# Optimization experiments

Hardware: AMD Instinct MI355X
Metric: run time of the kernel (lower is better)

## Reference

```python
import jax, jax.numpy as jnp
import numpy as np

C_S = 128
C_T = 128
C_OUT = 128


def _proj(x, W, b):
    # 1x1x1 Conv3d == per-voxel linear over channel dim. x: [B, Cin, T, H, W]
    return jnp.einsum('oc,bcthw->bothw', W, x) + b[None, :, None, None, None]


def setup_inputs() -> dict:
    key = jax.random.key(0)
    ks = jax.random.split(key, 12)
    B, T, H, W = 4, 4, 32, 32
    spatial_features = jax.random.normal(ks[0], (B, T, C_S, H, W), dtype=jnp.float32)
    temporal_features = jax.random.normal(ks[1], (B, C_T, T, H, W), dtype=jnp.float32)
    def w(k, o, i):
        return jax.random.normal(k, (o, i), dtype=jnp.float32) * (i ** -0.5)
    return {
        'spatial_features': spatial_features,
        'temporal_features': temporal_features,
        'Wq': w(ks[2], C_OUT, C_S), 'bq': jnp.zeros((C_OUT,), jnp.float32),
        'Wk': w(ks[3], C_OUT, C_T), 'bk': jnp.zeros((C_OUT,), jnp.float32),
        'Wv': w(ks[4], C_OUT, C_T), 'bv': jnp.zeros((C_OUT,), jnp.float32),
        'Wo': w(ks[5], C_OUT, C_OUT), 'bo': jnp.zeros((C_OUT,), jnp.float32),
    }


def reference(spatial_features, temporal_features, Wq, bq, Wk, bk, Wv, bv, Wo, bo):
    B, T, C_s, H, W = spatial_features.shape
    N = T * H * W
    scale = C_OUT ** -0.5
    # permute(0,2,1,3,4): [B, T, C_s, H, W] -> [B, C_s, T, H, W]
    x_s = jnp.transpose(spatial_features, (0, 2, 1, 3, 4))
    q = _proj(x_s, Wq, bq)                 # [B, C_out, T, H, W]
    k = _proj(temporal_features, Wk, bk)   # [B, C_out, T, H, W]
    v = _proj(temporal_features, Wv, bv)   # [B, C_out, T, H, W]
    Q = q.reshape(B, C_OUT, N).transpose(0, 2, 1)  # [B, N, C]
    K = k.reshape(B, C_OUT, N)                     # [B, C, N]
    V = v.reshape(B, C_OUT, N).transpose(0, 2, 1)  # [B, N, C]
    attn = jax.nn.softmax(jnp.einsum('bnc,bcm->bnm', Q, K) * scale, axis=2)  # [B, N, N]
    out = jnp.einsum('bnm,bmc->bnc', attn, V)      # [B, N, C]
    out = out.transpose(0, 2, 1).reshape(B, C_OUT, T, H, W)
    return _proj(out, Wo, bo)
```

## Files before the change

### kernel.cpp

```cpp
#include <hip/hip_runtime.h>
#include <cstddef>

#define NDIM 4096
#define SCALE_L2E 0.12751741843533886f
#define BIAS_L2E  11.541560327111707f

typedef _Float16 h8 __attribute__((ext_vector_type(8)));
typedef _Float16 h4 __attribute__((ext_vector_type(4)));
typedef _Float16 h2 __attribute__((ext_vector_type(2)));
typedef float    f4 __attribute__((ext_vector_type(4)));

__device__ __forceinline__ void gld_lds16(const void* g, void* l) {
    __builtin_amdgcn_global_load_lds(
        (const __attribute__((address_space(1))) void*)g,
        (__attribute__((address_space(3))) void*)l, 16, 0, 0);
}

__device__ __forceinline__ h8 cvt_w_frag(const float* wp) {
    const float4 u0 = *(const float4*)wp;
    const float4 u1 = *(const float4*)(wp + 4);
    h8 f;
    f[0]=(_Float16)u0.x; f[1]=(_Float16)u0.y; f[2]=(_Float16)u0.z; f[3]=(_Float16)u0.w;
    f[4]=(_Float16)u1.x; f[5]=(_Float16)u1.y; f[6]=(_Float16)u1.z; f[7]=(_Float16)u1.w;
    return f;
}

__global__ __launch_bounds__(256) void prep_w_kernel(
    const float* __restrict__ Wq, const float* __restrict__ Wk,
    const float* __restrict__ Wv, const float* __restrict__ Wo,
    _Float16* __restrict__ Whf)
{
    const int gid = blockIdx.x * 256 + threadIdx.x;
    const int mat = gid >> 11, rem = gid & 2047;
    const int ot = rem >> 8, ks = (rem >> 6) & 3, l = rem & 63;
    const float* src = mat == 0 ? Wq : mat == 1 ? Wk : mat == 2 ? Wv : Wo;
    const h8 f = cvt_w_frag(src + (size_t)(16 * ot + (l & 15)) * 128 + 32 * ks + 8 * (l >> 4));
    *(h8*)(Whf + (size_t)gid * 8) = f;
}

__global__ __launch_bounds__(256, 3) void proj_qkv_kernel(
    const float* __restrict__ spatial, const float* __restrict__ temporal,
    const _Float16* __restrict__ Whf,
    const float* __restrict__ bq, const float* __restrict__ bk,
    const float* __restrict__ bv,
    _Float16* __restrict__ Qh, _Float16* __restrict__ Kh, _Float16* __restrict__ Vt)
{
    __shared__ __align__(16) _Float16 Xl[32 * 136];
    const int tid = threadIdx.x;
    const int n0  = blockIdx.x * 32;
    const int b   = blockIdx.y;
    const int p   = blockIdx.z;
    const float* __restrict__ bias = (p == 0) ? bq : (p == 1) ? bk : bv;

    {
        const float* src; size_t rs;
        if (p == 0) { const int t = n0 >> 10, hw0 = n0 & 1023;
            src = spatial + (((size_t)(b * 4 + t) * 128) << 10) + hw0; rs = 1024; }
        else { src = temporal + ((size_t)(b * 128) << 12) + n0; rs = 4096; }
        #pragma unroll
        for (int i = 0; i < 2; ++i) {
            const int ii = tid + 256 * i;
            const int c2 = ii >> 3, j = ii & 7;
            const float4 v0 = *(const float4*)(src + (size_t)(2 * c2) * rs + 4 * j);
            const float4 v1 = *(const float4*)(src + (size_t)(2 * c2 + 1) * rs + 4 * j);
            const float a0[4] = {v0.x, v0.y, v0.z, v0.w};
            const float a1[4] = {v1.x, v1.y, v1.z, v1.w};
            #pragma unroll
            for (int u = 0; u < 4; ++u) {
                h2 pk; pk[0] = (_Float16)a0[u]; pk[1] = (_Float16)a1[u];
                *(h2*)&Xl[(4 * j + u) * 136 + 2 * c2] = pk;
            }
        }
    }
    __syncthreads();

    const int w = tid >> 6, lane = tid & 63, n16 = tid & 15, q4 = (tid >> 4) & 3;

    h8 wf[2][4];
    #pragma unroll
    for (int otl = 0; otl < 2; ++otl)
        #pragma unroll
        for (int ks = 0; ks < 4; ++ks)
            wf[otl][ks] = *(const h8*)(Whf + ((size_t)(((p * 8 + 2 * w + otl) * 4 + ks)) << 9)
                                           + lane * 8);
    h8 xf[2][4];
    #pragma unroll
    for (int ns = 0; ns < 2; ++ns)
        #pragma unroll
        for (int ks = 0; ks < 4; ++ks)
            xf[ns][ks] = *(const h8*)&Xl[(16 * ns + n16) * 136 + 32 * ks + 8 * q4];

    if (p < 2) {
        f4 acc[2][2];
        #pragma unroll
        for (int i = 0; i < 2; ++i) { acc[i][0] = (f4)0.0f; acc[i][1] = (f4)0.0f; }
        #pragma unroll
        for (int otl = 0; otl < 2; ++otl)
            #pragma unroll
            for (int ns = 0; ns < 2; ++ns)
                #pragma unroll
                for (int ks = 0; ks < 4; ++ks)
                    acc[otl][ns] = __builtin_amdgcn_mfma_f32_16x16x32_f16(
                        wf[otl][ks], xf[ns][ks], acc[otl][ns], 0, 0, 0);
        _Float16* __restrict__ dst = (p == 0) ? Qh : Kh;
        #pragma unroll
        for (int otl = 0; otl < 2; ++otl) {
            const float4 bb = *(const float4*)&bias[16 * (2 * w + otl) + 4 * q4];
            #pragma unroll
            for (int ns = 0; ns < 2; ++ns) {
                h4 r;
                r[0]=(_Float16)(acc[otl][ns][0]+bb.x); r[1]=(_Float16)(acc[otl][ns][1]+bb.y);
                r[2]=(_Float16)(acc[otl][ns][2]+bb.z); r[3]=(_Float16)(acc[otl][ns][3]+bb.w);
                *(h4*)(dst + ((size_t)b * NDIM + n0 + 16 * ns + n16) * 128
                           + 16 * (2 * w + otl) + 4 * q4) = r;
            }
        }
    } else {
        f4 acc[2][2];
        #pragma unroll
        for (int i = 0; i < 2; ++i) { acc[i][0] = (f4)0.0f; acc[i][1] = (f4)0.0f; }
        #pragma unroll
        for (int ns = 0; ns < 2; ++ns)
            #pragma unroll
            for (int otl = 0; otl < 2; ++otl)
                #pragma unroll
                for (int ks = 0; ks < 4; ++ks)
                    acc[ns][otl] = __builtin_amdgcn_mfma_f32_16x16x32_f16(
                        xf[ns][ks], wf[otl][ks], acc[ns][otl], 0, 0, 0);
        #pragma unroll
        for (int ns = 0; ns < 2; ++ns)
            #pragma unroll
            for (int otl = 0; otl < 2; ++otl) {
                const float bb = bias[16 * (2 * w + otl) + n16];
                h4 r;
                r[0]=(_Float16)(acc[ns][otl][0]+bb); r[1]=(_Float16)(acc[ns][otl][1]+bb);
                r[2]=(_Float16)(acc[ns][otl][2]+bb); r[3]=(_Float16)(acc[ns][otl][3]+bb);
                *(h4*)(Vt + ((size_t)(b * 128 + 16 * (2 * w + otl) + n16) << 12)
                          + n0 + 16 * ns + 4 * q4) = r;
            }
    }
}

__global__ __launch_bounds__(512, 4) void attn_kernel(
    const _Float16* __restrict__ Qh, const _Float16* __restrict__ Kh,
    const _Float16* __restrict__ Vt, _Float16* __restrict__ Opart,
    float* __restrict__ lpart)
{
    __shared__ __align__(16) _Float16 sh[30720];

    const int tid  = threadIdx.x;
    const int w    = tid >> 6, lane = tid & 63;
    const int g    = w >> 1,  p    = w & 1;
    const int n16  = lane & 15, q4 = lane >> 4;

    const int id = blockIdx.x + 32 * blockIdx.y + 128 * blockIdx.z;
    const int pi = (id & 7) + 8 * (id >> 8);
    const int qt = (id >> 3) & 31;
    const int hf = pi & 3, b = pi >> 2;
    const int n0 = qt * 128;
    const int mb = hf * 1024;

    const int kr = tid >> 4, kc = tid & 15;
    const _Float16* kg = Kh + ((size_t)b * NDIM + mb + kr) * 128
                            + 8 * (kc ^ (kr & 7));
    const int vr = tid >> 2, vc = tid & 3;
    const _Float16* vg = Vt + (((size_t)(b * 128 + vr)) << 12) + mb
                            + 8 * (vc ^ ((vr >> 1) & 3));
    const int ld = tid * 8;

    gld_lds16(kg, sh + ld);
    gld_lds16(vg, sh + 8192 + ld);
    kg += 32 * 128; vg += 32;

    h8 qf[2][4];
    {
        const _Float16* Qb = Qh + ((size_t)b * NDIM + n0 + 32 * g + n16) * 128;
        #pragma unroll
        for (int qs = 0; qs < 2; ++qs)
            #pragma unroll
            for (int ks = 0; ks < 4; ++ks)
                qf[qs][ks] = *(const h8*)(Qb + (size_t)(16 * qs) * 128 + 32 * ks + 8 * q4);
    }

    f4 oacc[2][4];
    #pragma unroll
    for (int i = 0; i < 2; ++i)
        #pragma unroll
        for (int j = 0; j < 4; ++j) oacc[i][j] = (f4)0.0f;
    float lsum[2] = {0.0f, 0.0f};

    const int kx   = (n16 & 7) << 3;
    const int krow = (16 * p + n16) * 128;

    for (int it = 0; it < 32; ++it) {
        __syncthreads();
        const int cur = it & 1;
        _Float16* __restrict__ Pb = sh + 20480 + cur * 5120;
        const _Float16* __restrict__ Pp = sh + 20480 + (cur ^ 1) * 5120;

        if (it < 31) {
            gld_lds16(kg, sh + (cur ^ 1) * 4096 + ld);
            gld_lds16(vg, sh + 8192 + ((it + 1) % 3) * 4096 + ld);
            kg += 32 * 128; vg += 32;
        }

        if (it > 0) {
            const _Float16* __restrict__ VP = sh + 8192 + ((it - 1) % 3) * 4096;
            h8 pf[2], vf[4];
            #pragma unroll
            for (int qs = 0; qs < 2; ++qs)
                pf[qs] = *(const h8*)&Pp[(32 * g + 16 * qs + n16) * 40 + 8 * q4];
            #pragma unroll
            for (int ct = 0; ct < 4; ++ct) {
                const int r = 64 * p + 16 * ct + n16;
                vf[ct] = *(const h8*)&VP[r * 32 + 8 * (q4 ^ ((r >> 1) & 3))];
            }
            __builtin_amdgcn_s_setprio(1);
            #pragma unroll
            for (int qs = 0; qs < 2; ++qs)
                #pragma unroll
                for (int ct = 0; ct < 4; ++ct)
                    oacc[qs][ct] = __builtin_amdgcn_mfma_f32_16x16x32_f16(
                        pf[qs], vf[ct], oacc[qs][ct], 0, 0, 0);
            __builtin_amdgcn_s_setprio(0);
        }

        f4 sacc[2];
        sacc[0] = (f4)0.0f; sacc[1] = (f4)0.0f;
        {
            const _Float16* __restrict__ KB = sh + cur * 4096;
            h8 kf[4];
            #pragma unroll
            for (int ks = 0; ks < 4; ++ks)
                kf[ks] = *(const h8*)&KB[krow + ((32 * ks + 8 * q4) ^ kx)];
            __builtin_amdgcn_s_setprio(1);
            #pragma unroll
            for (int ks = 0; ks < 4; ++ks)
                #pragma unroll
                for (int qs = 0; qs < 2; ++qs)
                    sacc[qs] = __builtin_amdgcn_mfma_f32_16x16x32_f16(
                        kf[ks], qf[qs][ks], sacc[qs], 0, 0, 0);
            __builtin_amdgcn_s_setprio(0);
        }

        #pragma unroll
        for (int qs = 0; qs < 2; ++qs) {
            h4 pk;
            #pragma unroll
            for (int r = 0; r < 4; ++r) {
                const float e = __builtin_amdgcn_exp2f(fmaf(sacc[qs][r], SCALE_L2E, -BIAS_L2E));
                lsum[qs] += e;
                pk[r] = (_Float16)e;
            }
            *(h4*)&Pb[(32 * g + 16 * qs + n16) * 40 + 16 * p + 4 * q4] = pk;
        }
    }

    __syncthreads();
    {
        const _Float16* __restrict__ Pp = sh + 20480 + 5120;
        const _Float16* __restrict__ VP = sh + 8192 + 1 * 4096;
        h8 pf[2], vf[4];
        #pragma unroll
        for (int qs = 0; qs < 2; ++qs)
            pf[qs] = *(const h8*)&Pp[(32 * g + 16 * qs + n16) * 40 + 8 * q4];
        #pragma unroll
        for (int ct = 0; ct < 4; ++ct) {
            const int r = 64 * p + 16 * ct + n16;
            vf[ct] = *(const h8*)&VP[r * 32 + 8 * (q4 ^ ((r >> 1) & 3))];
        }
        #pragma unroll
        for (int qs = 0; qs < 2; ++qs)
            #pragma unroll
            for (int ct = 0; ct < 4; ++ct)
                oacc[qs][ct] = __builtin_amdgcn_mfma_f32_16x16x32_f16(
                    pf[qs], vf[ct], oacc[qs][ct], 0, 0, 0);
    }

    #pragma unroll
    for (int qs = 0; qs < 2; ++qs) {
        lsum[qs] += __shfl_xor(lsum[qs], 16, 64);
        lsum[qs] += __shfl_xor(lsum[qs], 32, 64);
    }
    if (q4 == 0) {
        float* lb = lpart + ((size_t)((hf * 2 + p) * 4 + b)) * NDIM + n0 + 32 * g;
        #pragma unroll
        for (int qs = 0; qs < 2; ++qs) lb[16 * qs + n16] = lsum[qs];
    }

    __syncthreads();
    #pragma unroll
    for (int qs = 0; qs < 2; ++qs)
        #pragma unroll
        for (int ct = 0; ct < 4; ++ct)
            #pragma unroll
            for (int r = 0; r < 4; ++r)
                sh[(32 * g + 16 * qs + 4 * q4 + r) * 136 + 64 * p + 16 * ct + n16] =
                    (_Float16)oacc[qs][ct][r];
    __syncthreads();
    const size_t ob = ((size_t)(hf * 4 + b) * NDIM + n0) * 128;
    #pragma unroll
    for (int i = 0; i < 4; ++i) {
        const int ii  = tid + 512 * i;
        const int row = ii >> 4, c8 = (ii & 15) * 8;
        *(int4*)(Opart + ob + (size_t)row * 128 + c8) = *(const int4*)&sh[row * 136 + c8];
    }
}

__global__ __launch_bounds__(256, 2) void proj_final_kernel(
    const _Float16* __restrict__ Opart, const float* __restrict__ lpart,
    const _Float16* __restrict__ Whf, const float* __restrict__ bo,
    float* __restrict__ out)
{
    __shared__ __align__(16) _Float16 Xl[32 * 136];
    __shared__ float lrow[32];
    __shared__ __align__(16) float Ofin[128 * 36];
    const int tid = threadIdx.x;
    const int n0  = blockIdx.x * 32;
    const int b   = blockIdx.y;

    if (tid < 32) {
        float l = 0.0f;
        #pragma unroll
        for (int h8i = 0; h8i < 8; ++h8i)
            l += lpart[((size_t)(h8i * 4 + b)) * NDIM + n0 + tid];
        lrow[tid] = 1.0f / l;
    }
    float vals[2][8];
    int rows[2], c8s[2];
    #pragma unroll
    for (int i = 0; i < 2; ++i) {
        const int ii = tid + 256 * i;
        rows[i] = ii >> 4; c8s[i] = (ii & 15) * 8;
        #pragma unroll
        for (int j = 0; j < 8; ++j) vals[i][j] = 0.0f;
        #pragma unroll
        for (int hf = 0; hf < 4; ++hf) {
            const h8 o = *(const h8*)(Opart + ((size_t)(hf * 4 + b) * NDIM + n0 + rows[i]) * 128
                                      + c8s[i]);
            #pragma unroll
            for (int j = 0; j < 8; ++j) vals[i][j] += (float)o[j];
        }
    }
    __syncthreads();
    #pragma unroll
    for (int i = 0; i < 2; ++i) {
        const float linv = lrow[rows[i]];
        h8 r;
        #pragma unroll
        for (int j = 0; j < 8; ++j) r[j] = (_Float16)(vals[i][j] * linv);
        *(h8*)&Xl[rows[i] * 136 + c8s[i]] = r;
    }
    __syncthreads();

    const int w = tid >> 6, lane = tid & 63, n16 = tid & 15, q4 = (tid >> 4) & 3;

    h8 wf[2][4];
    #pragma unroll
    for (int otl = 0; otl < 2; ++otl)
        #pragma unroll
        for (int ks = 0; ks < 4; ++ks)
            wf[otl][ks] = *(const h8*)(Whf + ((size_t)(((3 * 8 + 2 * w + otl) * 4 + ks)) << 9)
                                           + lane * 8);
    h8 xf[2][4];
    #pragma unroll
    for (int ns = 0; ns < 2; ++ns)
        #pragma unroll
        for (int ks = 0; ks < 4; ++ks)
            xf[ns][ks] = *(const h8*)&Xl[(16 * ns + n16) * 136 + 32 * ks + 8 * q4];

    f4 acc[2][2];
    #pragma unroll
    for (int i = 0; i < 2; ++i) { acc[i][0] = (f4)0.0f; acc[i][1] = (f4)0.0f; }
    #pragma unroll
    for (int otl = 0; otl < 2; ++otl)
        #pragma unroll
        for (int ns = 0; ns < 2; ++ns)
            #pragma unroll
            for (int ks = 0; ks < 4; ++ks)
                acc[otl][ns] = __builtin_amdgcn_mfma_f32_16x16x32_f16(
                    wf[otl][ks], xf[ns][ks], acc[otl][ns], 0, 0, 0);

    #pragma unroll
    for (int otl = 0; otl < 2; ++otl) {
        const float4 bb = *(const float4*)&bo[16 * (2 * w + otl) + 4 * q4];
        const float bias[4] = {bb.x, bb.y, bb.z, bb.w};
        #pragma unroll
        for (int ns = 0; ns < 2; ++ns)
            #pragma unroll
            for (int r = 0; r < 4; ++r)
                Ofin[(16 * (2 * w + otl) + 4 * q4 + r) * 36 + 16 * ns + n16] =
                    acc[otl][ns][r] + bias[r];
    }
    __syncthreads();
    #pragma unroll
    for (int i = 0; i < 4; ++i) {
        const int ii  = tid + 256 * i;
        const int row = ii >> 3, j = ii & 7;
        *(float4*)(out + (((size_t)(b * 128 + row)) << 12) + n0 + 4 * j) =
            *(const float4*)&Ofin[row * 36 + 4 * j];
    }
}

extern "C" void kernel_launch(void* const* d_in, const int* in_sizes, int n_in,
                              void* d_out, int out_size, void* d_ws, size_t ws_size,
                              hipStream_t stream)
{
    const float* spatial  = (const float*)d_in[0];
    const float* temporal = (const float*)d_in[1];
    const float* Wq = (const float*)d_in[2];
    const float* bq = (const float*)d_in[3];
    const float* Wk = (const float*)d_in[4];
    const float* bk = (const float*)d_in[5];
    const float* Wv = (const float*)d_in[6];
    const float* bv = (const float*)d_in[7];
    const float* Wo = (const float*)d_in[8];
    const float* bo = (const float*)d_in[9];

    char* ws = (char*)d_ws;
    _Float16* Qh    = (_Float16*)(ws);
    _Float16* Kh    = (_Float16*)(ws + (4u  << 20));
    _Float16* Vt    = (_Float16*)(ws + (8u  << 20));
    _Float16* Opart = (_Float16*)(ws + (12u << 20));
    float*    lpart = (float*)   (ws + (28u << 20));
    _Float16* Whf   = (_Float16*)(ws + (28u << 20) + (512u << 10));

    prep_w_kernel<<<32, 256, 0, stream>>>(Wq, Wk, Wv, Wo, Whf);
    proj_qkv_kernel<<<dim3(128, 4, 3), 256, 0, stream>>>(
        spatial, temporal, Whf, bq, bk, bv, Qh, Kh, Vt);
    attn_kernel<<<dim3(32, 4, 4), 512, 0, stream>>>(Qh, Kh, Vt, Opart, lpart);
    proj_final_kernel<<<dim3(128, 4), 256, 0, stream>>>(Opart, lpart, Whf, bo,
                                                        (float*)d_out);
}
```

Measured before the change: 139.4 us.

## Warp-specialize attention: QK/softmax waves and PV waves run concurrently

Splits the eight waves of the attention block into two roles. Waves 0-3 compute S = K·Q and the exp, and write P to LDS. Waves 4-7 consume the previous tile's P with V and accumulate O. Each wave now covers 64 query rows instead of 32, which doubles its register accumulators: four Q fragments per wave for the QK side and 4x4 oacc tiles for the PV side. The aim is to overlap the exp work with the PV MFMAs across waves. The cost is higher register pressure under the (512,4) launch bounds and barrier counts that must match between the two branches.

```diff
diff --git a/kernel.cpp b/kernel.cpp
--- a/kernel.cpp
+++ b/kernel.cpp
@@ -150,7 +150,6 @@
 
     const int tid  = threadIdx.x;
     const int w    = tid >> 6, lane = tid & 63;
-    const int g    = w >> 1,  p    = w & 1;
     const int n16  = lane & 15, q4 = lane >> 4;
 
     const int id = blockIdx.x + 32 * blockIdx.y + 128 * blockIdx.z;
@@ -172,132 +171,148 @@
     gld_lds16(vg, sh + 8192 + ld);
     kg += 32 * 128; vg += 32;
 
-    h8 qf[2][4];
-    {
-        const _Float16* Qb = Qh + ((size_t)b * NDIM + n0 + 32 * g + n16) * 128;
-        #pragma unroll
-        for (int qs = 0; qs < 2; ++qs)
-            #pragma unroll
-            for (int ks = 0; ks < 4; ++ks)
-                qf[qs][ks] = *(const h8*)(Qb + (size_t)(16 * qs) * 128 + 32 * ks + 8 * q4);
-    }
-
-    f4 oacc[2][4];
-    #pragma unroll
-    for (int i = 0; i < 2; ++i)
-        #pragma unroll
-        for (int j = 0; j < 4; ++j) oacc[i][j] = (f4)0.0f;
-    float lsum[2] = {0.0f, 0.0f};
-
-    const int kx   = (n16 & 7) << 3;
-    const int krow = (16 * p + n16) * 128;
-
-    for (int it = 0; it < 32; ++it) {
-        __syncthreads();
-        const int cur = it & 1;
-        _Float16* __restrict__ Pb = sh + 20480 + cur * 5120;
-        const _Float16* __restrict__ Pp = sh + 20480 + (cur ^ 1) * 5120;
-
-        if (it < 31) {
-            gld_lds16(kg, sh + (cur ^ 1) * 4096 + ld);
-            gld_lds16(vg, sh + 8192 + ((it + 1) % 3) * 4096 + ld);
-            kg += 32 * 128; vg += 32;
-        }
-
-        if (it > 0) {
-            const _Float16* __restrict__ VP = sh + 8192 + ((it - 1) % 3) * 4096;
-            h8 pf[2], vf[4];
-            #pragma unroll
-            for (int qs = 0; qs < 2; ++qs)
-                pf[qs] = *(const h8*)&Pp[(32 * g + 16 * qs + n16) * 40 + 8 * q4];
+    const int rw = w & 3;
+    const int g  = rw >> 1, p = rw & 1;
+
+    if (w < 4) {
+        h8 qf[4][4];
+        {
+            const _Float16* Qb = Qh + ((size_t)b * NDIM + n0 + 64 * g + n16) * 128;
+            #pragma unroll
+            for (int qs = 0; qs < 4; ++qs)
+                #pragma unroll
+                for (int ks = 0; ks < 4; ++ks)
+                    qf[qs][ks] = *(const h8*)(Qb + (size_t)(16 * qs) * 128 + 32 * ks + 8 * q4);
+        }
+        float lsum[4] = {0.0f, 0.0f, 0.0f, 0.0f};
+        const int kx   = (n16 & 7) << 3;
+        const int krow = (16 * p + n16) * 128;
+        int vnxt = 1;
+
+        for (int it = 0; it < 32; ++it) {
+            __syncthreads();
+            const int cur = it & 1;
+            if (it < 31) {
+                gld_lds16(kg, sh + (cur ^ 1) * 4096 + ld);
+                gld_lds16(vg, sh + 8192 + vnxt * 4096 + ld);
+                kg += 32 * 128; vg += 32;
+                vnxt = vnxt == 2 ? 0 : vnxt + 1;
+            }
+            f4 sacc[4];
+            #pragma unroll
+            for (int qs = 0; qs < 4; ++qs) sacc[qs] = (f4)0.0f;
+            {
+                const _Float16* __restrict__ KB = sh + cur * 4096;
+                h8 kf[4];
+                #pragma unroll
+                for (int ks = 0; ks < 4; ++ks)
+                    kf[ks] = *(const h8*)&KB[krow + ((32 * ks + 8 * q4) ^ kx)];
+                __builtin_amdgcn_s_setprio(1);
+                #pragma unroll
+                for (int ks = 0; ks < 4; ++ks)
+                    #pragma unroll
+                    for (int qs = 0; qs < 4; ++qs)
+                        sacc[qs] = __builtin_amdgcn_mfma_f32_16x16x32_f16(
+                            kf[ks], qf[qs][ks], sacc[qs], 0, 0, 0);
+                __builtin_amdgcn_s_setprio(0);
+            }
+            _Float16* __restrict__ Pb = sh + 20480 + cur * 5120;
+            #pragma unroll
+            for (int qs = 0; qs < 4; ++qs) {
+                h4 pk;
+                #pragma unroll
+                for (int r = 0; r < 4; ++r) {
+                    const float e = __builtin_amdgcn_exp2f(
+                        fmaf(sacc[qs][r], SCALE_L2E, -BIAS_L2E));
+                    lsum[qs] += e;
+                    pk[r] = (_Float16)e;
+                }
+                *(h4*)&Pb[(64 * g + 16 * qs + n16) * 40 + 16 * p + 4 * q4] = pk;
+            }
+        }
+        __syncthreads();
+        #pragma unroll
+        for (int qs = 0; qs < 4; ++qs) {
+            lsum[qs] += __shfl_xor(lsum[qs], 16, 64);
+            lsum[qs] += __shfl_xor(lsum[qs], 32, 64);
+        }
+        if (q4 == 0) {
+            float* lb = lpart + ((size_t)((hf * 2 + p) * 4 + b)) * NDIM + n0 + 64 * g;
+            #pragma unroll
+            for (int qs = 0; qs < 4; ++qs) lb[16 * qs + n16] = lsum[qs];
+        }
+        __syncthreads();
+        __syncthreads();
+    } else {
+        f4 oacc[4][4];
+        #pragma unroll
+        for (int i = 0; i < 4; ++i)
+            #pragma unroll
+            for (int j = 0; j < 4; ++j) oacc[i][j] = (f4)0.0f;
+        int vnxt = 1, vprv = 0;
+
+        for (int it = 0; it < 32; ++it) {
+            __syncthreads();
+            const int cur = it & 1;
+            if (it < 31) {
+                gld_lds16(kg, sh + (cur ^ 1) * 4096 + ld);
+                gld_lds16(vg, sh + 8192 + vnxt * 4096 + ld);
+                kg += 32 * 128; vg += 32;
+                vnxt = vnxt == 2 ? 0 : vnxt + 1;
+            }
+            if (it > 0) {
+                const _Float16* __restrict__ Pp = sh + 20480 + (cur ^ 1) * 5120;
+                const _Float16* __restrict__ VP = sh + 8192 + vprv * 4096;
+                h8 vf[4];
+                #pragma unroll
+                for (int ct = 0; ct < 4; ++ct) {
+                    const int r = 64 * p + 16 * ct + n16;
+                    vf[ct] = *(const h8*)&VP[r * 32 + 8 * (q4 ^ ((r >> 1) & 3))];
+                }
+                __builtin_amdgcn_s_setprio(1);
+                #pragma unroll
+                for (int qs = 0; qs < 4; ++qs) {
+                    const h8 pf = *(const h8*)&Pp[(64 * g + 16 * qs + n16) * 40 + 8 * q4];
+                    #pragma unroll
+                    for (int ct = 0; ct < 4; ++ct)
+                        oacc[qs][ct] = __builtin_amdgcn_mfma_f32_16x16x32_f16(
+                            pf, vf[ct], oacc[qs][ct], 0, 0, 0);
+                }
+                __builtin_amdgcn_s_setprio(0);
+                vprv = vprv == 2 ? 0 : vprv + 1;
+            }
+        }
+        __syncthreads();
+        {
+            const _Float16* __restrict__ Pp = sh + 20480 + 5120;
+            const _Float16* __restrict__ VP = sh + 8192 + 4096;
+            h8 vf[4];
             #pragma unroll
             for (int ct = 0; ct < 4; ++ct) {
                 const int r = 64 * p + 16 * ct + n16;
                 vf[ct] = *(const h8*)&VP[r * 32 + 8 * (q4 ^ ((r >> 1) & 3))];
             }
-            __builtin_amdgcn_s_setprio(1);
-            #pragma unroll
-            for (int qs = 0; qs < 2; ++qs)
+            #pragma unroll
+            for (int qs = 0; qs < 4; ++qs) {
+                const h8 pf = *(const h8*)&Pp[(64 * g + 16 * qs + n16) * 40 + 8 * q4];
                 #pragma unroll
                 for (int ct = 0; ct < 4; ++ct)
                     oacc[qs][ct] = __builtin_amdgcn_mfma_f32_16x16x32_f16(
-                        pf[qs], vf[ct], oacc[qs][ct], 0, 0, 0);
-            __builtin_amdgcn_s_setprio(0);
-        }
-
-        f4 sacc[2];
-        sacc[0] = (f4)0.0f; sacc[1] = (f4)0.0f;
-        {
-            const _Float16* __restrict__ KB = sh + cur * 4096;
-            h8 kf[4];
-            #pragma unroll
-            for (int ks = 0; ks < 4; ++ks)
-                kf[ks] = *(const h8*)&KB[krow + ((32 * ks + 8 * q4) ^ kx)];
-            __builtin_amdgcn_s_setprio(1);
-            #pragma unroll
-            for (int ks = 0; ks < 4; ++ks)
-                #pragma unroll
-                for (int qs = 0; qs < 2; ++qs)
-                    sacc[qs] = __builtin_amdgcn_mfma_f32_16x16x32_f16(
-                        kf[ks], qf[qs][ks], sacc[qs], 0, 0, 0);
-            __builtin_amdgcn_s_setprio(0);
-        }
-
-        #pragma unroll
-        for (int qs = 0; qs < 2; ++qs) {
-            h4 pk;
-            #pragma unroll
-            for (int r = 0; r < 4; ++r) {
-                const float e = __builtin_amdgcn_exp2f(fmaf(sacc[qs][r], SCALE_L2E, -BIAS_L2E));
-                lsum[qs] += e;
-                pk[r] = (_Float16)e;
-            }
-            *(h4*)&Pb[(32 * g + 16 * qs + n16) * 40 + 16 * p + 4 * q4] = pk;
-        }
-    }
-
-    __syncthreads();
-    {
-        const _Float16* __restrict__ Pp = sh + 20480 + 5120;
-        const _Float16* __restrict__ VP = sh + 8192 + 1 * 4096;
-        h8 pf[2], vf[4];
-        #pragma unroll
-        for (int qs = 0; qs < 2; ++qs)
-            pf[qs] = *(const h8*)&Pp[(32 * g + 16 * qs + n16) * 40 + 8 * q4];
-        #pragma unroll
-        for (int ct = 0; ct < 4; ++ct) {
-            const int r = 64 * p + 16 * ct + n16;
-            vf[ct] = *(const h8*)&VP[r * 32 + 8 * (q4 ^ ((r >> 1) & 3))];
-        }
-        #pragma unroll
-        for (int qs = 0; qs < 2; ++qs)
+                        pf, vf[ct], oacc[qs][ct], 0, 0, 0);
+            }
+        }
+        __syncthreads();
+        #pragma unroll
+        for (int qs = 0; qs < 4; ++qs)
             #pragma unroll
             for (int ct = 0; ct < 4; ++ct)
-                oacc[qs][ct] = __builtin_amdgcn_mfma_f32_16x16x32_f16(
-                    pf[qs], vf[ct], oacc[qs][ct], 0, 0, 0);
-    }
-
-    #pragma unroll
-    for (int qs = 0; qs < 2; ++qs) {
-        lsum[qs] += __shfl_xor(lsum[qs], 16, 64);
-        lsum[qs] += __shfl_xor(lsum[qs], 32, 64);
-    }
-    if (q4 == 0) {
-        float* lb = lpart + ((size_t)((hf * 2 + p) * 4 + b)) * NDIM + n0 + 32 * g;
-        #pragma unroll
-        for (int qs = 0; qs < 2; ++qs) lb[16 * qs + n16] = lsum[qs];
-    }
-
-    __syncthreads();
-    #pragma unroll
-    for (int qs = 0; qs < 2; ++qs)
-        #pragma unroll
-        for (int ct = 0; ct < 4; ++ct)
-            #pragma unroll
-            for (int r = 0; r < 4; ++r)
-                sh[(32 * g + 16 * qs + 4 * q4 + r) * 136 + 64 * p + 16 * ct + n16] =
-                    (_Float16)oacc[qs][ct][r];
-    __syncthreads();
+                #pragma unroll
+                for (int r = 0; r < 4; ++r)
+                    sh[(64 * g + 16 * qs + 4 * q4 + r) * 136 + 64 * p + 16 * ct + n16] =
+                        (_Float16)oacc[qs][ct][r];
+        __syncthreads();
+    }
+
     const size_t ob = ((size_t)(hf * 4 + b) * NDIM + n0) * 128;
     #pragma unroll
     for (int i = 0; i < 4; ++i) {
```

Result: faster. 134.1 us (-3.8%).
